# Kernel optimization log

Measured on AMD Instinct MI355X. Metric: run time of the kernel, lower is better.

## Reference

```python
import jax, jax.numpy as jnp
import numpy as np

LEAKY_SLOPE = 0.01  # torch nn.LeakyReLU default

def leaky_relu(x):
    return jnp.where(x >= 0, x, LEAKY_SLOPE * x)

def setup_inputs() -> dict:
    key = jax.random.key(0)
    ks = jax.random.split(key, 11)
    B, F, C_IN, H, K, D = 2048, 512, 3, 64, 8, 128  # batch, features, expand, layer_conf[0], bucket_num, bucket_dim
    ASR, MM, OUT = 128, 768, 256
    proj_in = ASR + MM + F * D
    inp = {
        "stat_features": jax.random.uniform(ks[0], (B, F), dtype=jnp.float32),
        "asr_embeddings": jax.random.normal(ks[1], (B, ASR), dtype=jnp.float32),
        "mm_embeddings": jax.random.normal(ks[2], (B, MM), dtype=jnp.float32),
        "linear1_w": jax.random.normal(ks[3], (F, C_IN, H), dtype=jnp.float32) * (1.0 / np.sqrt(C_IN)),
        "linear1_b": jax.random.normal(ks[4], (F, 1, H), dtype=jnp.float32),
        "linear2_w": jax.random.normal(ks[5], (F, H, K), dtype=jnp.float32) * (1.0 / np.sqrt(H)),
        "linear2_b": jax.random.normal(ks[6], (F, 1, K), dtype=jnp.float32),
        "tau": jnp.ones((F, 1, K), dtype=jnp.float32),
        "emb": jax.random.normal(ks[7], (F, K, D), dtype=jnp.float32),
        "proj_w": jax.random.normal(ks[8], (OUT, proj_in), dtype=jnp.float32) * (1.0 / np.sqrt(proj_in)),
        "proj_b": jax.random.normal(ks[9], (OUT,), dtype=jnp.float32) * 0.01,
    }
    return inp

def reference(stat_features, asr_embeddings, mm_embeddings,
              linear1_w, linear1_b, linear2_w, linear2_b, tau, emb,
              proj_w, proj_b):
    # sanitize: NaN -> 0, negatives -> 0
    x = stat_features
    x = jnp.where(jnp.isnan(x) | (x < 0.0), 0.0, x)  # [B, F]

    # auto_dis: per-feature tiny MLP. x is expanded to 3 identical copies -> [B,F,1,3]
    # matmul with [F,3,H] == einsum over the 3 copies.
    B, F = x.shape
    x3 = jnp.broadcast_to(x[:, :, None], (B, F, 3))           # [B,F,3]
    h = jnp.einsum('bfc,fch->bfh', x3, linear1_w) + linear1_b[:, 0, :]  # [B,F,H]
    h = jnp.where(h >= 0, h, LEAKY_SLOPE * h)
    s = jnp.einsum('bfh,fhk->bfk', h, linear2_w) + linear2_b[:, 0, :]   # [B,F,K]
    s = jnp.where(s >= 0, s, LEAKY_SLOPE * s)
    s = s * tau[:, 0, :]
    p = jax.nn.softmax(s, axis=-1)                            # [B,F,K]
    y = jnp.einsum('bfk,fkd->bfd', p, emb)                    # [B,F,D]
    y = y.reshape(B, -1)                                      # [B, F*D] (fc = Identity)

    z = jnp.concatenate([asr_embeddings, mm_embeddings, y], axis=1)
    out = jax.nn.relu(z @ proj_w.T + proj_b)                  # [B, 256]
    return out
```

## Files before the change

### kernel.cpp

```cpp
#include <hip/hip_runtime.h>
#include <hip/hip_bf16.h>
#include <math.h>

#define LEAKY 0.01f
#define B_    2048
#define F_    512
#define H_    64
#define K_    8
#define D_    128
#define ASR_  128
#define MM_   768
#define OUT_  256
#define PROJ_IN 66432
#define ZK    4992
#define PK    4096
#define NSPLIT 8


typedef unsigned short u16;
typedef u16   u16x4 __attribute__((ext_vector_type(4)));
typedef u16   u16x8 __attribute__((ext_vector_type(8)));
typedef short s16x8 __attribute__((ext_vector_type(8)));
typedef float f32x4 __attribute__((ext_vector_type(4)));

__device__ __forceinline__ u16 f2bf(float x) {
  unsigned int u = __float_as_uint(x);
  u += 0x7fffu + ((u >> 16) & 1u);
  return (u16)(u >> 16);
}

#define W1S 65
#define W2S 516
#define PRODUCER_BLOCKS (1024 + 2048 + 224)

__global__ __launch_bounds__(256) void producer_kernel(
    const float* __restrict__ stat, const float* __restrict__ w1,
    const float* __restrict__ b1v, const float* __restrict__ w2,
    const float* __restrict__ b2v, const float* __restrict__ tauv,
    const float* __restrict__ pw, const float* __restrict__ emb,
    u16* __restrict__ P, u16* __restrict__ Wn) {
  __shared__ __align__(16) char smem[14688];
  const int bid = blockIdx.x;
  const int t = threadIdx.x;

  if (bid < 1024) {
    const int f0 = (bid & 127) * 4;
    const int b0 = (bid >> 7) * 256;
    float* s_w1s = (float*)(smem);
    float* s_b1  = (float*)(smem + 1040);
    float* s_w2  = (float*)(smem + 2080);
    float* s_b2  = (float*)(smem + 10336);
    float* s_tau = (float*)(smem + 10464);
    float* s_x   = (float*)(smem + 10592);
    {
      int fl = t >> 6, h = t & 63;
      const float* wf = w1 + (size_t)(f0 + fl) * 192;
      s_w1s[fl * W1S + h] = wf[h] + wf[64 + h] + wf[128 + h];
      s_b1[fl * W1S + h] = b1v[(size_t)(f0 + fl) * 64 + h];
    }
    for (int i = t; i < 4 * 512; i += 256) {
      int fl = i >> 9, idx = i & 511;
      s_w2[fl * W2S + idx] = w2[(size_t)(f0 + fl) * 512 + idx];
    }
    if (t < 32) {
      int fl = t >> 3, k = t & 7;
      s_b2[t]  = b2v[(f0 + fl) * 8 + k];
      s_tau[t] = tauv[(f0 + fl) * 8 + k];
    }
    for (int i = t; i < 1024; i += 256) {
      int r = i >> 2, j = i & 3;
      float v = stat[(size_t)(b0 + r) * F_ + f0 + j];
      s_x[i] = (v >= 0.f) ? v : 0.f;
    }
    __syncthreads();

    const int fl = t & 3, rb = t >> 2;
    float x[4];
    #pragma unroll
    for (int p = 0; p < 4; ++p) x[p] = s_x[(rb + 64 * p) * 4 + fl];
    float acc[4][8] = {{0.f}};
    const float* w1p = s_w1s + fl * W1S;
    const float* b1p = s_b1 + fl * W1S;
    const float* w2p = s_w2 + fl * W2S;
    #pragma unroll 8
    for (int i = 0; i < 64; ++i) {
      float wv = w1p[i], bv = b1p[i];
      float4 wa = *(const float4*)(w2p + i * 8);
      float4 wb = *(const float4*)(w2p + i * 8 + 4);
      #pragma unroll
      for (int p = 0; p < 4; ++p) {
        float h = fmaf(x[p], wv, bv);
        h = (h >= 0.f) ? h : LEAKY * h;
        acc[p][0] = fmaf(h, wa.x, acc[p][0]);
        acc[p][1] = fmaf(h, wa.y, acc[p][1]);
        acc[p][2] = fmaf(h, wa.z, acc[p][2]);
        acc[p][3] = fmaf(h, wa.w, acc[p][3]);
        acc[p][4] = fmaf(h, wb.x, acc[p][4]);
        acc[p][5] = fmaf(h, wb.y, acc[p][5]);
        acc[p][6] = fmaf(h, wb.z, acc[p][6]);
        acc[p][7] = fmaf(h, wb.w, acc[p][7]);
      }
    }
    #pragma unroll
    for (int p = 0; p < 4; ++p) {
      float s[K_];
      float m = -1e30f;
      #pragma unroll
      for (int k = 0; k < K_; ++k) {
        float v = acc[p][k] + s_b2[fl * 8 + k];
        v = (v >= 0.f) ? v : LEAKY * v;
        v *= s_tau[fl * 8 + k];
        s[k] = v;
        m = fmaxf(m, v);
      }
      float sum = 0.f;
      #pragma unroll
      for (int k = 0; k < K_; ++k) { s[k] = __expf(s[k] - m); sum += s[k]; }
      float inv = 1.f / sum;
      u16x8 hv;
      #pragma unroll
      for (int k = 0; k < K_; ++k) hv[k] = f2bf(s[k] * inv);
      *(u16x8*)(P + (size_t)(b0 + rb + 64 * p) * PK + (f0 + fl) * 8) = hv;
    }
  } else if (bid < 3072) {
    const int item = bid - 1024;
    const int f = item >> 2;
    const int o0 = (item & 3) * 64;
    float* s_emb = (float*)smem;
    for (int i = t; i < K_ * D_; i += 256) s_emb[i] = emb[(size_t)f * K_ * D_ + i];
    __syncthreads();
    const int orow = t >> 2, dc = t & 3;
    const float* src = pw + (size_t)(o0 + orow) * PROJ_IN + 896 + f * D_;
    float g[K_] = {0.f, 0.f, 0.f, 0.f, 0.f, 0.f, 0.f, 0.f};
    #pragma unroll
    for (int j = 0; j < 8; ++j) {
      const int d = dc * 4 + j * 16;
      float4 w = *(const float4*)(src + d);
      #pragma unroll
      for (int k = 0; k < K_; ++k) {
        float4 e = *(const float4*)(s_emb + k * D_ + d);
        g[k] = fmaf(w.x, e.x, g[k]);
        g[k] = fmaf(w.y, e.y, g[k]);
        g[k] = fmaf(w.z, e.z, g[k]);
        g[k] = fmaf(w.w, e.w, g[k]);
      }
    }
    #pragma unroll
    for (int k = 0; k < K_; ++k) {
      g[k] += __shfl_xor(g[k], 1);
      g[k] += __shfl_xor(g[k], 2);
    }
    if (dc == 0) {
      u16x8 hv;
      #pragma unroll
      for (int k = 0; k < K_; ++k) hv[k] = f2bf(g[k]);
      *(u16x8*)(Wn + (size_t)(o0 + orow) * ZK + 896 + f * K_) = hv;
    }
  } else {
    const int item = bid - 3072;
    #pragma unroll
    for (int r = 0; r < 4; ++r) {
      int idx = item * 1024 + r * 256 + t;
      int o = idx / 896, j = idx % 896;
      Wn[(size_t)o * ZK + j] = f2bf(pw[(size_t)o * PROJ_IN + j]);
    }
  }
}

#define SAS 136
__global__ __launch_bounds__(256) void gemm_kernel(
    const float* __restrict__ asr, const float* __restrict__ mm,
    const u16* __restrict__ P, const u16* __restrict__ Wn,
    float* __restrict__ part) {
  const int bm0 = blockIdx.x * 64;
  const int bn0 = blockIdx.y * 64;
  const int kz  = blockIdx.z;
  const int it0 = kz * 5;
  const int itn = (kz == 7) ? 4 : 5;
  __shared__ u16 sA[64 * SAS];
  __shared__ u16 sB[64 * SAS];
  const int t = threadIdx.x;
  const int w = t >> 6, L = t & 63;
  const int l16 = L & 15, q8 = (L >> 4) * 8;
  const int wm = (w >> 1) * 32, wn = (w & 1) * 32;
  const int row = t >> 2, lk = t & 3;
  f32x4 acc[2][2] = {{{0.f,0.f,0.f,0.f},{0.f,0.f,0.f,0.f}},
                     {{0.f,0.f,0.f,0.f},{0.f,0.f,0.f,0.f}}};
  float4 fa[8];
  u16x8 pa[4];
  u16x8 wb[4];

#define LOAD_TILES(IT)                                                        \
  {                                                                           \
    const int k0_ = (IT) * 128;                                               \
    if (k0_ == 0) {                                                           \
      const float* s_ = asr + (size_t)(bm0 + row) * ASR_ + lk * 32;           \
      _Pragma("unroll")                                                       \
      for (int j_ = 0; j_ < 8; ++j_) fa[j_] = *(const float4*)(s_ + j_ * 4);  \
    } else if (k0_ < 896) {                                                   \
      const float* s_ = mm + (size_t)(bm0 + row) * MM_ + (k0_ - 128) + lk * 32;\
      _Pragma("unroll")                                                       \
      for (int j_ = 0; j_ < 8; ++j_) fa[j_] = *(const float4*)(s_ + j_ * 4);  \
    } else {                                                                  \
      const u16* s_ = P + (size_t)(bm0 + row) * PK + (k0_ - 896) + lk * 32;   \
      _Pragma("unroll")                                                       \
      for (int j_ = 0; j_ < 4; ++j_) pa[j_] = *(const u16x8*)(s_ + j_ * 8);   \
    }                                                                         \
    const u16* sb_ = Wn + (size_t)(bn0 + row) * ZK + k0_ + lk * 32;           \
    _Pragma("unroll")                                                         \
    for (int j_ = 0; j_ < 4; ++j_) wb[j_] = *(const u16x8*)(sb_ + j_ * 8);    \
  }

#define STORE_TILES(IT)                                                       \
  {                                                                           \
    if ((IT) * 128 < 896) {                                                   \
      _Pragma("unroll")                                                       \
      for (int j_ = 0; j_ < 8; ++j_) {                                        \
        u16x4 h_ = {f2bf(fa[j_].x), f2bf(fa[j_].y), f2bf(fa[j_].z),           \
                    f2bf(fa[j_].w)};                                          \
        *(u16x4*)&sA[row * SAS + lk * 32 + j_ * 4] = h_;                      \
      }                                                                       \
    } else {                                                                  \
      _Pragma("unroll")                                                       \
      for (int j_ = 0; j_ < 4; ++j_)                                          \
        *(u16x8*)&sA[row * SAS + lk * 32 + j_ * 8] = pa[j_];                  \
    }                                                                         \
    _Pragma("unroll")                                                         \
    for (int j_ = 0; j_ < 4; ++j_)                                            \
      *(u16x8*)&sB[row * SAS + lk * 32 + j_ * 8] = wb[j_];                    \
  }

  LOAD_TILES(it0);
  for (int it = it0; it < it0 + itn; ++it) {
    __syncthreads();
    STORE_TILES(it);
    __syncthreads();
    if (it + 1 < it0 + itn) LOAD_TILES(it + 1);
    #pragma unroll
    for (int ks = 0; ks < 4; ++ks) {
      s16x8 a0 = *(const s16x8*)&sA[(wm + l16) * SAS + ks * 32 + q8];
      s16x8 a1 = *(const s16x8*)&sA[(wm + 16 + l16) * SAS + ks * 32 + q8];
      s16x8 b0 = *(const s16x8*)&sB[(wn + l16) * SAS + ks * 32 + q8];
      s16x8 b1 = *(const s16x8*)&sB[(wn + 16 + l16) * SAS + ks * 32 + q8];
      acc[0][0] = __builtin_amdgcn_mfma_f32_16x16x32_bf16(a0, b0, acc[0][0], 0, 0, 0);
      acc[0][1] = __builtin_amdgcn_mfma_f32_16x16x32_bf16(a0, b1, acc[0][1], 0, 0, 0);
      acc[1][0] = __builtin_amdgcn_mfma_f32_16x16x32_bf16(a1, b0, acc[1][0], 0, 0, 0);
      acc[1][1] = __builtin_amdgcn_mfma_f32_16x16x32_bf16(a1, b1, acc[1][1], 0, 0, 0);
    }
  }
#undef LOAD_TILES
#undef STORE_TILES

  float* dst = part + (size_t)kz * B_ * OUT_;
  #pragma unroll
  for (int mf = 0; mf < 2; ++mf) {
    const int r0 = bm0 + wm + mf * 16 + (L >> 4) * 4;
    #pragma unroll
    for (int nf = 0; nf < 2; ++nf) {
      const int col = bn0 + wn + nf * 16 + l16;
      #pragma unroll
      for (int i = 0; i < 4; ++i)
        dst[(size_t)(r0 + i) * OUT_ + col] = acc[mf][nf][i];
    }
  }
}

__global__ __launch_bounds__(256) void combine_kernel(
    const float* __restrict__ part, const float* __restrict__ pb,
    float* __restrict__ out) {
  const int idx4 = (blockIdx.x * 256 + threadIdx.x) * 4;
  const int o = idx4 & (OUT_ - 1);
  float4 bv = *(const float4*)(pb + o);
  float4 r = bv;
  #pragma unroll
  for (int kz = 0; kz < NSPLIT; ++kz) {
    float4 a = *(const float4*)(part + (size_t)kz * B_ * OUT_ + idx4);
    r.x += a.x; r.y += a.y; r.z += a.z; r.w += a.w;
  }
  r.x = r.x > 0.f ? r.x : 0.f;
  r.y = r.y > 0.f ? r.y : 0.f;
  r.z = r.z > 0.f ? r.z : 0.f;
  r.w = r.w > 0.f ? r.w : 0.f;
  *(float4*)(out + idx4) = r;
}

extern "C" void kernel_launch(void* const* d_in, const int* in_sizes, int n_in,
                              void* d_out, int out_size, void* d_ws, size_t ws_size,
                              hipStream_t stream) {
  (void)in_sizes; (void)n_in; (void)out_size; (void)ws_size;
  const float* stat = (const float*)d_in[0];
  const float* asr  = (const float*)d_in[1];
  const float* mm   = (const float*)d_in[2];
  const float* w1   = (const float*)d_in[3];
  const float* b1   = (const float*)d_in[4];
  const float* w2   = (const float*)d_in[5];
  const float* b2   = (const float*)d_in[6];
  const float* tau  = (const float*)d_in[7];
  const float* emb  = (const float*)d_in[8];
  const float* pw   = (const float*)d_in[9];
  const float* pb   = (const float*)d_in[10];
  float* out = (float*)d_out;
  char* ws = (char*)d_ws;
  u16*   P    = (u16*)(ws);
  u16*   Wn   = (u16*)(ws + 16777216);
  float* part = (float*)(ws + 19333120);

  producer_kernel<<<PRODUCER_BLOCKS, 256, 0, stream>>>(
      stat, w1, b1, w2, b2, tau, pw, emb, P, Wn);
  gemm_kernel<<<dim3(B_ / 64, OUT_ / 64, NSPLIT), 256, 0, stream>>>(
      asr, mm, P, Wn, part);
  combine_kernel<<<B_ * OUT_ / 1024, 256, 0, stream>>>(part, pb, out);
}
```

Baseline: 171.5 us.

## Precast activations to bf16, store P feature-major, and halve GEMM K-tile

The producer kernel now also converts the asr/mm embeddings to a bf16 buffer A0, and writes the softmax probabilities in a feature-major layout (Pf[f][b][8]). The GEMM no longer converts fp32 to bf16 in its inner loop and uses a 64-wide K tile with half the registers per thread, doubling the iteration count. The per-feature MLP blocks each process 512 rows with one feature per wave, and the emb-projection blocks are placed first in the grid. The aim is to cut GEMM register pressure and conversion work, at the cost of an extra bf16 buffer write and strided 16-byte loads from the feature-major P.

```diff
diff --git a/kernel.cpp b/kernel.cpp
--- a/kernel.cpp
+++ b/kernel.cpp
@@ -13,7 +13,6 @@
 #define OUT_  256
 #define PROJ_IN 66432
 #define ZK    4992
-#define PK    4096
 #define NSPLIT 8
 
 
@@ -29,68 +28,102 @@
   return (u16)(u >> 16);
 }
 
-#define W1S 65
-#define W2S 516
-#define PRODUCER_BLOCKS (1024 + 2048 + 224)
+#define PRODUCER_BLOCKS (2048 + 512 + 896 + 224)
 
 __global__ __launch_bounds__(256) void producer_kernel(
     const float* __restrict__ stat, const float* __restrict__ w1,
     const float* __restrict__ b1v, const float* __restrict__ w2,
     const float* __restrict__ b2v, const float* __restrict__ tauv,
     const float* __restrict__ pw, const float* __restrict__ emb,
-    u16* __restrict__ P, u16* __restrict__ Wn) {
-  __shared__ __align__(16) char smem[14688];
+    const float* __restrict__ asr, const float* __restrict__ mm,
+    u16* __restrict__ A0, u16* __restrict__ Pf, u16* __restrict__ Wn) {
+  __shared__ __align__(16) char smem[20992];
   const int bid = blockIdx.x;
   const int t = threadIdx.x;
 
-  if (bid < 1024) {
-    const int f0 = (bid & 127) * 4;
-    const int b0 = (bid >> 7) * 256;
+  if (bid < 2048) {
+    const int f = bid >> 2;
+    const int o0 = (bid & 3) * 64;
+    float* s_emb = (float*)smem;
+    for (int i = t; i < K_ * D_; i += 256) s_emb[i] = emb[(size_t)f * K_ * D_ + i];
+    __syncthreads();
+    const int orow = t >> 2, dc = t & 3;
+    const float* src = pw + (size_t)(o0 + orow) * PROJ_IN + 896 + f * D_;
+    float g[K_] = {0.f, 0.f, 0.f, 0.f, 0.f, 0.f, 0.f, 0.f};
+    #pragma unroll
+    for (int j = 0; j < 8; ++j) {
+      const int d = dc * 4 + j * 16;
+      float4 w = *(const float4*)(src + d);
+      #pragma unroll
+      for (int k = 0; k < K_; ++k) {
+        float4 e = *(const float4*)(s_emb + k * D_ + d);
+        g[k] = fmaf(w.x, e.x, g[k]);
+        g[k] = fmaf(w.y, e.y, g[k]);
+        g[k] = fmaf(w.z, e.z, g[k]);
+        g[k] = fmaf(w.w, e.w, g[k]);
+      }
+    }
+    #pragma unroll
+    for (int k = 0; k < K_; ++k) {
+      g[k] += __shfl_xor(g[k], 1);
+      g[k] += __shfl_xor(g[k], 2);
+    }
+    if (dc == 0) {
+      u16x8 hv;
+      #pragma unroll
+      for (int k = 0; k < K_; ++k) hv[k] = f2bf(g[k]);
+      *(u16x8*)(Wn + (size_t)(o0 + orow) * ZK + 896 + f * K_) = hv;
+    }
+  } else if (bid < 2560) {
+    const int pb = bid - 2048;
+    const int f0 = (pb & 127) * 4;
+    const int b0 = (pb >> 7) * 512;
     float* s_w1s = (float*)(smem);
-    float* s_b1  = (float*)(smem + 1040);
-    float* s_w2  = (float*)(smem + 2080);
-    float* s_b2  = (float*)(smem + 10336);
-    float* s_tau = (float*)(smem + 10464);
-    float* s_x   = (float*)(smem + 10592);
+    float* s_b1  = (float*)(smem + 1024);
+    float* s_w2  = (float*)(smem + 2048);
+    float* s_b2  = (float*)(smem + 10240);
+    float* s_tau = (float*)(smem + 10368);
+    float* s_x   = (float*)(smem + 10496);
     {
       int fl = t >> 6, h = t & 63;
       const float* wf = w1 + (size_t)(f0 + fl) * 192;
-      s_w1s[fl * W1S + h] = wf[h] + wf[64 + h] + wf[128 + h];
-      s_b1[fl * W1S + h] = b1v[(size_t)(f0 + fl) * 64 + h];
+      s_w1s[fl * 64 + h] = wf[h] + wf[64 + h] + wf[128 + h];
+      s_b1[fl * 64 + h] = b1v[(size_t)(f0 + fl) * 64 + h];
     }
     for (int i = t; i < 4 * 512; i += 256) {
       int fl = i >> 9, idx = i & 511;
-      s_w2[fl * W2S + idx] = w2[(size_t)(f0 + fl) * 512 + idx];
+      s_w2[fl * 512 + idx] = w2[(size_t)(f0 + fl) * 512 + idx];
     }
     if (t < 32) {
-      int fl = t >> 3, k = t & 7;
-      s_b2[t]  = b2v[(f0 + fl) * 8 + k];
-      s_tau[t] = tauv[(f0 + fl) * 8 + k];
-    }
-    for (int i = t; i < 1024; i += 256) {
-      int r = i >> 2, j = i & 3;
-      float v = stat[(size_t)(b0 + r) * F_ + f0 + j];
-      s_x[i] = (v >= 0.f) ? v : 0.f;
+      s_b2[t]  = b2v[f0 * 8 + t];
+      s_tau[t] = tauv[f0 * 8 + t];
+    }
+    for (int p = 0; p < 8; ++p) {
+      int i = p * 256 + t;
+      int r = i >> 2, fl = i & 3;
+      float v = stat[(size_t)(b0 + r) * F_ + f0 + fl];
+      s_x[r * 5 + fl] = (v >= 0.f) ? v : 0.f;
     }
     __syncthreads();
 
-    const int fl = t & 3, rb = t >> 2;
-    float x[4];
-    #pragma unroll
-    for (int p = 0; p < 4; ++p) x[p] = s_x[(rb + 64 * p) * 4 + fl];
-    float acc[4][8] = {{0.f}};
-    const float* w1p = s_w1s + fl * W1S;
-    const float* b1p = s_b1 + fl * W1S;
-    const float* w2p = s_w2 + fl * W2S;
-    #pragma unroll 8
+    const int w = t >> 6;
+    const int lane = t & 63;
+    const float* w1p = s_w1s + w * 64;
+    const float* b1p = s_b1 + w * 64;
+    const float* w2p = s_w2 + w * 512;
+    float x[8];
+    #pragma unroll
+    for (int p = 0; p < 8; ++p) x[p] = s_x[(lane + 64 * p) * 5 + w];
+    float acc[8][8] = {{0.f}};
+    #pragma unroll 4
     for (int i = 0; i < 64; ++i) {
       float wv = w1p[i], bv = b1p[i];
       float4 wa = *(const float4*)(w2p + i * 8);
       float4 wb = *(const float4*)(w2p + i * 8 + 4);
       #pragma unroll
-      for (int p = 0; p < 4; ++p) {
-        float h = fmaf(x[p], wv, bv);
-        h = (h >= 0.f) ? h : LEAKY * h;
+      for (int p = 0; p < 8; ++p) {
+        float h0 = fmaf(x[p], wv, bv);
+        float h = fmaf(LEAKY, fminf(h0, 0.f), fmaxf(h0, 0.f));
         acc[p][0] = fmaf(h, wa.x, acc[p][0]);
         acc[p][1] = fmaf(h, wa.y, acc[p][1]);
         acc[p][2] = fmaf(h, wa.z, acc[p][2]);
@@ -102,14 +135,14 @@
       }
     }
     #pragma unroll
-    for (int p = 0; p < 4; ++p) {
+    for (int p = 0; p < 8; ++p) {
       float s[K_];
       float m = -1e30f;
       #pragma unroll
       for (int k = 0; k < K_; ++k) {
-        float v = acc[p][k] + s_b2[fl * 8 + k];
+        float v = acc[p][k] + s_b2[w * 8 + k];
         v = (v >= 0.f) ? v : LEAKY * v;
-        v *= s_tau[fl * 8 + k];
+        v *= s_tau[w * 8 + k];
         s[k] = v;
         m = fmaxf(m, v);
       }
@@ -120,63 +153,43 @@
       u16x8 hv;
       #pragma unroll
       for (int k = 0; k < K_; ++k) hv[k] = f2bf(s[k] * inv);
-      *(u16x8*)(P + (size_t)(b0 + rb + 64 * p) * PK + (f0 + fl) * 8) = hv;
-    }
-  } else if (bid < 3072) {
-    const int item = bid - 1024;
-    const int f = item >> 2;
-    const int o0 = (item & 3) * 64;
-    float* s_emb = (float*)smem;
-    for (int i = t; i < K_ * D_; i += 256) s_emb[i] = emb[(size_t)f * K_ * D_ + i];
-    __syncthreads();
-    const int orow = t >> 2, dc = t & 3;
-    const float* src = pw + (size_t)(o0 + orow) * PROJ_IN + 896 + f * D_;
-    float g[K_] = {0.f, 0.f, 0.f, 0.f, 0.f, 0.f, 0.f, 0.f};
-    #pragma unroll
-    for (int j = 0; j < 8; ++j) {
-      const int d = dc * 4 + j * 16;
-      float4 w = *(const float4*)(src + d);
-      #pragma unroll
-      for (int k = 0; k < K_; ++k) {
-        float4 e = *(const float4*)(s_emb + k * D_ + d);
-        g[k] = fmaf(w.x, e.x, g[k]);
-        g[k] = fmaf(w.y, e.y, g[k]);
-        g[k] = fmaf(w.z, e.z, g[k]);
-        g[k] = fmaf(w.w, e.w, g[k]);
-      }
-    }
-    #pragma unroll
-    for (int k = 0; k < K_; ++k) {
-      g[k] += __shfl_xor(g[k], 1);
-      g[k] += __shfl_xor(g[k], 2);
-    }
-    if (dc == 0) {
-      u16x8 hv;
-      #pragma unroll
-      for (int k = 0; k < K_; ++k) hv[k] = f2bf(g[k]);
-      *(u16x8*)(Wn + (size_t)(o0 + orow) * ZK + 896 + f * K_) = hv;
-    }
+      *(u16x8*)(Pf + ((size_t)(f0 + w) * B_ + b0 + lane + 64 * p) * 8) = hv;
+    }
+  } else if (bid < 3456) {
+    const int item = bid - 2560;
+    const int cidx = item * 256 + t;
+    const int r = cidx / 112, c = cidx % 112;
+    float4 v0, v1;
+    if (c < 16) {
+      const float* s = asr + (size_t)r * ASR_ + c * 8;
+      v0 = *(const float4*)(s); v1 = *(const float4*)(s + 4);
+    } else {
+      const float* s = mm + (size_t)r * MM_ + (c - 16) * 8;
+      v0 = *(const float4*)(s); v1 = *(const float4*)(s + 4);
+    }
+    u16x8 hv = {f2bf(v0.x), f2bf(v0.y), f2bf(v0.z), f2bf(v0.w),
+                f2bf(v1.x), f2bf(v1.y), f2bf(v1.z), f2bf(v1.w)};
+    *(u16x8*)(A0 + (size_t)r * 896 + c * 8) = hv;
   } else {
-    const int item = bid - 3072;
-    #pragma unroll
-    for (int r = 0; r < 4; ++r) {
-      int idx = item * 1024 + r * 256 + t;
+    const int item = bid - 3456;
+    #pragma unroll
+    for (int rr = 0; rr < 4; ++rr) {
+      int idx = item * 1024 + rr * 256 + t;
       int o = idx / 896, j = idx % 896;
       Wn[(size_t)o * ZK + j] = f2bf(pw[(size_t)o * PROJ_IN + j]);
     }
   }
 }
 
-#define SAS 136
+#define SAS 72
 __global__ __launch_bounds__(256) void gemm_kernel(
-    const float* __restrict__ asr, const float* __restrict__ mm,
-    const u16* __restrict__ P, const u16* __restrict__ Wn,
-    float* __restrict__ part) {
+    const u16* __restrict__ A0, const u16* __restrict__ Pf,
+    const u16* __restrict__ Wn, float* __restrict__ part) {
   const int bm0 = blockIdx.x * 64;
   const int bn0 = blockIdx.y * 64;
   const int kz  = blockIdx.z;
-  const int it0 = kz * 5;
-  const int itn = (kz == 7) ? 4 : 5;
+  const int it0 = kz * 10;
+  const int itn = (kz == 7) ? 8 : 10;
   __shared__ u16 sA[64 * SAS];
   __shared__ u16 sB[64 * SAS];
   const int t = threadIdx.x;
@@ -186,58 +199,41 @@
   const int row = t >> 2, lk = t & 3;
   f32x4 acc[2][2] = {{{0.f,0.f,0.f,0.f},{0.f,0.f,0.f,0.f}},
                      {{0.f,0.f,0.f,0.f},{0.f,0.f,0.f,0.f}}};
-  float4 fa[8];
-  u16x8 pa[4];
-  u16x8 wb[4];
+  u16x8 ra[2], rb[2];
 
 #define LOAD_TILES(IT)                                                        \
   {                                                                           \
-    const int k0_ = (IT) * 128;                                               \
-    if (k0_ == 0) {                                                           \
-      const float* s_ = asr + (size_t)(bm0 + row) * ASR_ + lk * 32;           \
-      _Pragma("unroll")                                                       \
-      for (int j_ = 0; j_ < 8; ++j_) fa[j_] = *(const float4*)(s_ + j_ * 4);  \
-    } else if (k0_ < 896) {                                                   \
-      const float* s_ = mm + (size_t)(bm0 + row) * MM_ + (k0_ - 128) + lk * 32;\
-      _Pragma("unroll")                                                       \
-      for (int j_ = 0; j_ < 8; ++j_) fa[j_] = *(const float4*)(s_ + j_ * 4);  \
+    const int k0_ = (IT) * 64;                                                \
+    if (k0_ < 896) {                                                          \
+      const u16* s_ = A0 + (size_t)(bm0 + row) * 896 + k0_ + lk * 8;          \
+      ra[0] = *(const u16x8*)(s_);                                            \
+      ra[1] = *(const u16x8*)(s_ + 32);                                       \
     } else {                                                                  \
-      const u16* s_ = P + (size_t)(bm0 + row) * PK + (k0_ - 896) + lk * 32;   \
-      _Pragma("unroll")                                                       \
-      for (int j_ = 0; j_ < 4; ++j_) pa[j_] = *(const u16x8*)(s_ + j_ * 8);   \
+      const int fb_ = (k0_ - 896) >> 3;                                       \
+      ra[0] = *(const u16x8*)(Pf + ((size_t)(fb_ + lk) * B_ + bm0 + row) * 8);\
+      ra[1] = *(const u16x8*)(Pf + ((size_t)(fb_ + 4 + lk) * B_ + bm0 + row) * 8);\
     }                                                                         \
-    const u16* sb_ = Wn + (size_t)(bn0 + row) * ZK + k0_ + lk * 32;           \
-    _Pragma("unroll")                                                         \
-    for (int j_ = 0; j_ < 4; ++j_) wb[j_] = *(const u16x8*)(sb_ + j_ * 8);    \
-  }
-
-#define STORE_TILES(IT)                                                       \
+    const u16* sb_ = Wn + (size_t)(bn0 + row) * ZK + k0_ + lk * 8;            \
+    rb[0] = *(const u16x8*)(sb_);                                             \
+    rb[1] = *(const u16x8*)(sb_ + 32);                                        \
+  }
+
+#define STORE_TILES()                                                         \
   {                                                                           \
-    if ((IT) * 128 < 896) {                                                   \
-      _Pragma("unroll")                                                       \
-      for (int j_ = 0; j_ < 8; ++j_) {                                        \
-        u16x4 h_ = {f2bf(fa[j_].x), f2bf(fa[j_].y), f2bf(fa[j_].z),           \
-                    f2bf(fa[j_].w)};                                          \
-        *(u16x4*)&sA[row * SAS + lk * 32 + j_ * 4] = h_;                      \
-      }                                                                       \
-    } else {                                                                  \
-      _Pragma("unroll")                                                       \
-      for (int j_ = 0; j_ < 4; ++j_)                                          \
-        *(u16x8*)&sA[row * SAS + lk * 32 + j_ * 8] = pa[j_];                  \
-    }                                                                         \
-    _Pragma("unroll")                                                         \
-    for (int j_ = 0; j_ < 4; ++j_)                                            \
-      *(u16x8*)&sB[row * SAS + lk * 32 + j_ * 8] = wb[j_];                    \
+    *(u16x8*)&sA[row * SAS + lk * 8]      = ra[0];                            \
+    *(u16x8*)&sA[row * SAS + lk * 8 + 32] = ra[1];                            \
+    *(u16x8*)&sB[row * SAS + lk * 8]      = rb[0];                            \
+    *(u16x8*)&sB[row * SAS + lk * 8 + 32] = rb[1];                            \
   }
 
   LOAD_TILES(it0);
   for (int it = it0; it < it0 + itn; ++it) {
     __syncthreads();
-    STORE_TILES(it);
+    STORE_TILES();
     __syncthreads();
     if (it + 1 < it0 + itn) LOAD_TILES(it + 1);
     #pragma unroll
-    for (int ks = 0; ks < 4; ++ks) {
+    for (int ks = 0; ks < 2; ++ks) {
       s16x8 a0 = *(const s16x8*)&sA[(wm + l16) * SAS + ks * 32 + q8];
       s16x8 a1 = *(const s16x8*)&sA[(wm + 16 + l16) * SAS + ks * 32 + q8];
       s16x8 b0 = *(const s16x8*)&sB[(wn + l16) * SAS + ks * 32 + q8];
@@ -301,13 +297,14 @@
   const float* pb   = (const float*)d_in[10];
   float* out = (float*)d_out;
   char* ws = (char*)d_ws;
-  u16*   P    = (u16*)(ws);
-  u16*   Wn   = (u16*)(ws + 16777216);
-  float* part = (float*)(ws + 19333120);
+  u16*   A0   = (u16*)(ws);
+  u16*   Pf   = (u16*)(ws + 3670016);
+  u16*   Wn   = (u16*)(ws + 20447232);
+  float* part = (float*)(ws + 23003136);
 
   producer_kernel<<<PRODUCER_BLOCKS, 256, 0, stream>>>(
-      stat, w1, b1, w2, b2, tau, pw, emb, P, Wn);
+      stat, w1, b1, w2, b2, tau, pw, emb, asr, mm, A0, Pf, Wn);
   gemm_kernel<<<dim3(B_ / 64, OUT_ / 64, NSPLIT), 256, 0, stream>>>(
-      asr, mm, P, Wn, part);
+      A0, Pf, Wn, part);
   combine_kernel<<<B_ * OUT_ / 1024, 256, 0, stream>>>(part, pb, out);
 }
```

After: 172.8 us. Within noise of the previous version (+0.8%).
